# Kernel tuning notes

Hardware: AMD Instinct MI355X
Metric: run time of the kernel (lower is better)

## Reference

```python
import jax, jax.numpy as jnp
import numpy as np

H, C = 4, 32            # heads, per-head out channels -> H*C = 128
NEG = jnp.float32(-1e9) # stand-in for -inf mask (keeps grads finite)
NUM_LOC = 15            # self.num_locations hardcoded to 15


def _tconv(x, src, dst, ea, Wq, bq, Wk, bk, Wv, bv, We, Ws, bs, Wb):
    # PyG TransformerConv(beta=True, concat=True, edge_dim=1)
    N = x.shape[0]
    q = (x @ Wq + bq).reshape(N, H, C)
    k = (x @ Wk + bk).reshape(N, H, C)
    v = (x @ Wv + bv).reshape(N, H, C)
    e = (ea @ We).reshape(-1, H, C)  # edge embedding [E,H,C]
    kj = k[src] + e
    alpha = jnp.einsum('ehc,ehc->eh', q[dst], kj) / jnp.sqrt(jnp.float32(C))
    # scatter-softmax over incoming edges of each dst node
    amax = jax.ops.segment_max(alpha, dst, num_segments=N)
    ex = jnp.exp(alpha - amax[dst])
    den = jax.ops.segment_sum(ex, dst, num_segments=N)
    w = ex / (den[dst] + 1e-16)
    out = jax.ops.segment_sum((v[src] + e) * w[..., None], dst, num_segments=N).reshape(N, H * C)
    xr = x @ Ws + bs  # lin_skip
    beta = jax.nn.sigmoid(jnp.concatenate([out, xr, out - xr], axis=-1) @ Wb)  # [N,1]
    return beta * xr + (1.0 - beta) * out


def _bn(x, g, b):
    # BatchNorm1d in training mode (batch statistics, biased var)
    m = x.mean(0)
    v = ((x - m) ** 2).mean(0)
    return (x - m) * jax.lax.rsqrt(v + 1e-5) * g + b


def _forward_core(fa, edge_index, active_mask):
    (node_type, requests, latency,
     c0_Wq, c0_bq, c0_Wk, c0_bk, c0_Wv, c0_bv, c0_We, c0_Ws, c0_bs, c0_Wb,
     t0_W, t0_b, bn0_g, bn0_b,
     cs_Wq, cs_bq, cs_Wk, cs_bk, cs_Wv, cs_bv, cs_We, cs_Ws, cs_bs, cs_Wb,
     ts_W, ts_b, bns_g, bns_b,
     emb_W1, emb_b1, emb_W2, emb_b2, emb_W3, emb_b3,
     rem_W, rem_b, add_W, add_b) = fa
    src, dst = edge_index[0], edge_index[1]
    ea = latency[:, None]                      # edge_attr [E,1]
    x = jnp.stack([node_type, requests], axis=1)  # [N,2]
    # NetworkGraphEmbeddingConstructor: conv1 + 4 stacked conv/linear/bn blocks
    x = _tconv(x, src, dst, ea, c0_Wq, c0_bq, c0_Wk, c0_bk, c0_Wv, c0_bv, c0_We, c0_Ws, c0_bs, c0_Wb)
    x = _bn(jax.nn.relu(x @ t0_W + t0_b), bn0_g, bn0_b)
    for i in range(4):
        x = _tconv(x, src, dst, ea, cs_Wq[i], cs_bq[i], cs_Wk[i], cs_bk[i], cs_Wv[i], cs_bv[i], cs_We[i], cs_Ws[i], cs_bs[i], cs_Wb[i])
        x = _bn(jax.nn.relu(x @ ts_W[i] + ts_b[i]), bns_g[i], bns_b[i])
    # embedding_transformation MLP
    x = jax.nn.relu(x @ emb_W1 + emb_b1)
    x = jax.nn.relu(x @ emb_W2 + emb_b2)
    x = x @ emb_W3 + emb_b3                    # [N,64]
    # sampling head (batch_index=None branch)
    N = x.shape[0]
    maskf = jnp.where(active_mask == 1, jnp.float32(0.0), NEG)
    loc = jnp.arange(N) < NUM_LOC
    remove_mask = jnp.where(loc, jnp.where(maskf == 0.0, NEG, jnp.float32(0.0)), maskf)
    logits1 = (x @ rem_W + rem_b)[:, 0] + remove_mask
    k1, k2 = jax.random.split(jax.random.key(42))
    a1 = jnp.argmax(logits1 + jax.random.gumbel(k1, (N,), logits1.dtype))  # Categorical sample
    mask2 = maskf.at[a1].set(0.0)
    t = jnp.tanh(x[a1] @ add_W + add_b)        # [64]
    logits2 = x @ t + mask2
    a2 = jnp.argmax(logits2 + jax.random.gumbel(k2, (N,), logits2.dtype))
    log_probs = jnp.stack([jax.nn.log_softmax(logits1)[a1], jax.nn.log_softmax(logits2)[a2]])
    return jnp.stack([logits1, logits2]), jnp.stack([a1, a2]), log_probs


def setup_inputs() -> dict:
    N, E = 50000, 400000
    F, HC, EMB, L = 2, 128, 32, 4
    key = jax.random.key(0)
    kit = iter(jax.random.split(key, 64))
    def w(shape, s=0.1):
        return jax.random.normal(next(kit), shape, jnp.float32) * s
    return {
        'node_type': w((N,), 1.0),
        'requests': jax.random.uniform(next(kit), (N,), jnp.float32),
        'latency': jax.random.uniform(next(kit), (E,), jnp.float32),
        'edge_index': jax.random.randint(next(kit), (2, E), 0, N, jnp.int32),
        'active_mask': jax.random.randint(next(kit), (N,), 0, 2, jnp.int32),
        'c0_Wq': w((F, HC)), 'c0_bq': w((HC,)),
        'c0_Wk': w((F, HC)), 'c0_bk': w((HC,)),
        'c0_Wv': w((F, HC)), 'c0_bv': w((HC,)),
        'c0_We': w((1, HC)),
        'c0_Ws': w((F, HC)), 'c0_bs': w((HC,)),
        'c0_Wb': w((3 * HC, 1)),
        't0_W': w((HC, EMB)), 't0_b': w((EMB,)),
        'bn0_g': jnp.ones((EMB,), jnp.float32), 'bn0_b': jnp.zeros((EMB,), jnp.float32),
        'cs_Wq': w((L, EMB, HC)), 'cs_bq': w((L, HC)),
        'cs_Wk': w((L, EMB, HC)), 'cs_bk': w((L, HC)),
        'cs_Wv': w((L, EMB, HC)), 'cs_bv': w((L, HC)),
        'cs_We': w((L, 1, HC)),
        'cs_Ws': w((L, EMB, HC)), 'cs_bs': w((L, HC)),
        'cs_Wb': w((L, 3 * HC, 1)),
        'ts_W': w((L, HC, EMB)), 'ts_b': w((L, EMB)),
        'bns_g': jnp.ones((L, EMB), jnp.float32), 'bns_b': jnp.zeros((L, EMB), jnp.float32),
        'emb_W1': w((EMB, 128)), 'emb_b1': w((128,)),
        'emb_W2': w((128, 64)), 'emb_b2': w((64,)),
        'emb_W3': w((64, 64)), 'emb_b3': w((64,)),
        'rem_W': w((64, 1)), 'rem_b': w((1,)),
        'add_W': w((64, 64)), 'add_b': w((64,)),
    }


def reference(node_type, requests, latency, edge_index, active_mask,
              c0_Wq, c0_bq, c0_Wk, c0_bk, c0_Wv, c0_bv, c0_We, c0_Ws, c0_bs, c0_Wb,
              t0_W, t0_b, bn0_g, bn0_b,
              cs_Wq, cs_bq, cs_Wk, cs_bk, cs_Wv, cs_bv, cs_We, cs_Ws, cs_bs, cs_Wb,
              ts_W, ts_b, bns_g, bns_b,
              emb_W1, emb_b1, emb_W2, emb_b2, emb_W3, emb_b3,
              rem_W, rem_b, add_W, add_b):
    fa = (node_type, requests, latency,
          c0_Wq, c0_bq, c0_Wk, c0_bk, c0_Wv, c0_bv, c0_We, c0_Ws, c0_bs, c0_Wb,
          t0_W, t0_b, bn0_g, bn0_b,
          cs_Wq, cs_bq, cs_Wk, cs_bk, cs_Wv, cs_bv, cs_We, cs_Ws, cs_bs, cs_Wb,
          ts_W, ts_b, bns_g, bns_b,
          emb_W1, emb_b1, emb_W2, emb_b2, emb_W3, emb_b3,
          rem_W, rem_b, add_W, add_b)
    return _forward_core(fa, edge_index, active_mask)
```

## Files before the change

kernel.cpp:

```cpp
#include <hip/hip_runtime.h>
#include <hip/hip_fp16.h>
#include <cstdint>
#include <math.h>

typedef _Float16 h2 __attribute__((ext_vector_type(2)));

__device__ __forceinline__ h2 f2h2(float a, float b) {
    h2 r; r.x = (_Float16)a; r.y = (_Float16)b; return r;
}
__device__ __forceinline__ float fdot2f(h2 a, h2 b, float c) {
    return __builtin_amdgcn_fdot2(a, b, c, false);
}

union f4h {
    float4 f;
    h2 h[4];
    __half2 u[4];
};

__device__ __forceinline__ uint32_t rotl32(uint32_t x, uint32_t n) {
    return (x << n) | (x >> (32u - n));
}

__device__ __forceinline__ void tf2x32(uint32_t k0, uint32_t k1,
                                       uint32_t x0, uint32_t x1,
                                       uint32_t& o0, uint32_t& o1) {
    uint32_t k2 = k0 ^ k1 ^ 0x1BD11BDAu;
    x0 += k0; x1 += k1;
    x0 += x1; x1 = rotl32(x1, 13); x1 ^= x0;
    x0 += x1; x1 = rotl32(x1, 15); x1 ^= x0;
    x0 += x1; x1 = rotl32(x1, 26); x1 ^= x0;
    x0 += x1; x1 = rotl32(x1, 6);  x1 ^= x0;
    x0 += k1; x1 += k2 + 1u;
    x0 += x1; x1 = rotl32(x1, 17); x1 ^= x0;
    x0 += x1; x1 = rotl32(x1, 29); x1 ^= x0;
    x0 += x1; x1 = rotl32(x1, 16); x1 ^= x0;
    x0 += x1; x1 = rotl32(x1, 24); x1 ^= x0;
    x0 += k2; x1 += k0 + 2u;
    x0 += x1; x1 = rotl32(x1, 13); x1 ^= x0;
    x0 += x1; x1 = rotl32(x1, 15); x1 ^= x0;
    x0 += x1; x1 = rotl32(x1, 26); x1 ^= x0;
    x0 += x1; x1 = rotl32(x1, 6);  x1 ^= x0;
    x0 += k0; x1 += k1 + 3u;
    x0 += x1; x1 = rotl32(x1, 17); x1 ^= x0;
    x0 += x1; x1 = rotl32(x1, 29); x1 ^= x0;
    x0 += x1; x1 = rotl32(x1, 16); x1 ^= x0;
    x0 += x1; x1 = rotl32(x1, 24); x1 ^= x0;
    x0 += k1; x1 += k2 + 4u;
    x0 += x1; x1 = rotl32(x1, 13); x1 ^= x0;
    x0 += x1; x1 = rotl32(x1, 15); x1 ^= x0;
    x0 += x1; x1 = rotl32(x1, 26); x1 ^= x0;
    x0 += x1; x1 = rotl32(x1, 6);  x1 ^= x0;
    x0 += k2; x1 += k0 + 5u;
    o0 = x0; o1 = x1;
}

__device__ float gumbel_at(int n, int which, int N) {
    uint32_t a0, a1, b0, b1;
    tf2x32(0u, 42u, 0u, 2u, a0, a1);
    tf2x32(0u, 42u, 1u, 3u, b0, b1);
    uint32_t gk0 = which ? a1 : a0;
    uint32_t gk1 = which ? b1 : b0;
    int half = N >> 1;
    uint32_t o0, o1, bits;
    if (n < half) { tf2x32(gk0, gk1, (uint32_t)n, (uint32_t)(n + half), o0, o1); bits = o0; }
    else          { tf2x32(gk0, gk1, (uint32_t)(n - half), (uint32_t)n, o0, o1); bits = o1; }
    float f = __uint_as_float((bits >> 9) | 0x3F800000u) - 1.0f;
    float u = fmaxf(1.17549435e-38f, f);
    return -logf(-logf(u));
}

__device__ __forceinline__ uint32_t fmono(float f) {
    uint32_t b = __float_as_uint(f);
    return (b & 0x80000000u) ? ~b : (b | 0x80000000u);
}
__device__ __forceinline__ float funmono(uint32_t u) {
    uint32_t b = (u & 0x80000000u) ? (u & 0x7FFFFFFFu) : ~u;
    return __uint_as_float(b);
}

#define NEGF (-1e9f)
#define ATTNGRID 2048

__global__ void k_hist(const int* __restrict__ dstp, int* __restrict__ deg, int E) {
    int e = blockIdx.x * 256 + threadIdx.x;
    if (e < E) atomicAdd(&deg[dstp[e]], 1);
}

__global__ void k_scan1(const int* __restrict__ deg, int* __restrict__ bsum, int N) {
    __shared__ int s[256];
    int i = blockIdx.x * 256 + threadIdx.x;
    s[threadIdx.x] = (i < N) ? deg[i] : 0;
    __syncthreads();
    for (int st = 128; st > 0; st >>= 1) {
        if (threadIdx.x < st) s[threadIdx.x] += s[threadIdx.x + st];
        __syncthreads();
    }
    if (threadIdx.x == 0) bsum[blockIdx.x] = s[0];
}

__global__ void k_scan2(int* __restrict__ bsum, int nb) {
    __shared__ int s[256];
    int i = threadIdx.x;
    int v = (i < nb) ? bsum[i] : 0;
    s[i] = v;
    __syncthreads();
    for (int st = 1; st < 256; st <<= 1) {
        int t = (i >= st) ? s[i - st] : 0;
        __syncthreads();
        s[i] += t;
        __syncthreads();
    }
    if (i < nb) bsum[i] = s[i] - v;
}

__global__ void k_scan3(const int* __restrict__ deg, const int* __restrict__ bsum,
                        int* __restrict__ rowptr, int* __restrict__ cursor, int N) {
    __shared__ int s[256];
    int i = blockIdx.x * 256 + threadIdx.x;
    int v = (i < N) ? deg[i] : 0;
    s[threadIdx.x] = v;
    __syncthreads();
    for (int st = 1; st < 256; st <<= 1) {
        int t = (threadIdx.x >= st) ? s[threadIdx.x - st] : 0;
        __syncthreads();
        s[threadIdx.x] += t;
        __syncthreads();
    }
    int excl = s[threadIdx.x] - v + bsum[blockIdx.x];
    if (i < N) { rowptr[i] = excl; cursor[i] = excl; }
}

__global__ void k_fill(const int* __restrict__ dstp, const int* __restrict__ srcp,
                       const float* __restrict__ lat, int* __restrict__ cursor,
                       int2* __restrict__ srclat, int E) {
    int e = blockIdx.x * 256 + threadIdx.x;
    if (e < E) {
        int pos = atomicAdd(&cursor[dstp[e]], 1);
        srclat[pos] = make_int2(srcp[e], __float_as_int(lat[e]));
    }
}

__global__ __launch_bounds__(512, 4) void k_qkvr(
        const float* __restrict__ xin, const float* __restrict__ nt,
        const float* __restrict__ rq, int din, int N,
        const float* __restrict__ Wq, const float* __restrict__ bq,
        const float* __restrict__ Wk, const float* __restrict__ bk,
        const float* __restrict__ Wv, const float* __restrict__ bv,
        const float* __restrict__ Ws, const float* __restrict__ bs,
        const double* __restrict__ SUM, const double* __restrict__ SUMSQ,
        const float* __restrict__ bng, const float* __restrict__ bnb,
        int applyBN,
        __half* __restrict__ Q, __half* __restrict__ KV, __half* __restrict__ R) {
    __shared__ h2 w2[4][16 * 128];
    __shared__ float bias[4][128];
    __shared__ h2 xs2[32][17];
    __shared__ float sscale[32], sshift[32];
    int t = threadIdx.x;
    int dpCount = din >> 1;
    for (int i = t; i < dpCount * 128; i += 512) {
        int dp = i >> 7, j = i & 127;
        w2[0][i] = f2h2(Wq[(size_t)(2 * dp) * 128 + j], Wq[(size_t)(2 * dp + 1) * 128 + j]);
        w2[1][i] = f2h2(Wk[(size_t)(2 * dp) * 128 + j], Wk[(size_t)(2 * dp + 1) * 128 + j]);
        w2[2][i] = f2h2(Wv[(size_t)(2 * dp) * 128 + j], Wv[(size_t)(2 * dp + 1) * 128 + j]);
        w2[3][i] = f2h2(Ws[(size_t)(2 * dp) * 128 + j], Ws[(size_t)(2 * dp + 1) * 128 + j]);
    }
    if (t < 128) {
        bias[0][t] = bq[t]; bias[1][t] = bk[t]; bias[2][t] = bv[t]; bias[3][t] = bs[t];
    }
    if (t < 32) {
        if (applyBN) {
            double m = SUM[t] / N;
            double v = SUMSQ[t] / N - m * m;
            float inv = rsqrtf((float)v + 1e-5f);
            float sc = inv * bng[t];
            sscale[t] = sc;
            sshift[t] = bnb[t] - (float)m * sc;
        } else {
            sscale[t] = 1.f; sshift[t] = 0.f;
        }
    }
    int quad = t & 31;
    int sub = t >> 5;
    int dpsh = (din == 32) ? 4 : 0;
    int tiles = (N + 31) >> 5;
    for (int tile = blockIdx.x; tile < tiles; tile += gridDim.x) {
        int base = tile << 5;
        __syncthreads();
        for (int i = t; i < 32 * dpCount; i += 512) {
            int nl = i >> dpsh, dp = i & (dpCount - 1);
            int nn = base + nl;
            float x0 = 0.f, x1 = 0.f;
            if (nn < N) {
                if (din == 2) { x0 = nt[nn]; x1 = rq[nn]; }
                else {
                    x0 = xin[(size_t)nn * din + 2 * dp];
                    x1 = xin[(size_t)nn * din + 2 * dp + 1];
                }
            }
            x0 = x0 * sscale[2 * dp] + sshift[2 * dp];
            x1 = x1 * sscale[2 * dp + 1] + sshift[2 * dp + 1];
            xs2[nl][dp] = f2h2(x0, x1);
        }
        __syncthreads();
        float acc[4][2][4];
#pragma unroll
        for (int m = 0; m < 4; ++m)
#pragma unroll
            for (int k = 0; k < 2; ++k)
#pragma unroll
                for (int c = 0; c < 4; ++c) acc[m][k][c] = bias[m][quad * 4 + c];
        for (int dp = 0; dp < dpCount; ++dp) {
            h2 xv0 = xs2[sub * 2 + 0][dp];
            h2 xv1 = xs2[sub * 2 + 1][dp];
#pragma unroll
            for (int m = 0; m < 4; ++m) {
                const h2* wp = &w2[m][dp * 128 + quad * 4];
                h2 wa = wp[0], wb = wp[1], wc = wp[2], wd = wp[3];
                acc[m][0][0] = fdot2f(xv0, wa, acc[m][0][0]);
                acc[m][0][1] = fdot2f(xv0, wb, acc[m][0][1]);
                acc[m][0][2] = fdot2f(xv0, wc, acc[m][0][2]);
                acc[m][0][3] = fdot2f(xv0, wd, acc[m][0][3]);
                acc[m][1][0] = fdot2f(xv1, wa, acc[m][1][0]);
                acc[m][1][1] = fdot2f(xv1, wb, acc[m][1][1]);
                acc[m][1][2] = fdot2f(xv1, wc, acc[m][1][2]);
                acc[m][1][3] = fdot2f(xv1, wd, acc[m][1][3]);
            }
        }
#pragma unroll
        for (int k = 0; k < 2; ++k) {
            int n = base + sub * 2 + k;
            if (n < N) {
                *(__half2*)&Q[(size_t)n * 128 + quad * 4 + 0] =
                    __floats2half2_rn(acc[0][k][0], acc[0][k][1]);
                *(__half2*)&Q[(size_t)n * 128 + quad * 4 + 2] =
                    __floats2half2_rn(acc[0][k][2], acc[0][k][3]);
                *(__half2*)&KV[(size_t)n * 256 + quad * 4 + 0] =
                    __floats2half2_rn(acc[1][k][0], acc[1][k][1]);
                *(__half2*)&KV[(size_t)n * 256 + quad * 4 + 2] =
                    __floats2half2_rn(acc[1][k][2], acc[1][k][3]);
                *(__half2*)&KV[(size_t)n * 256 + 128 + quad * 4 + 0] =
                    __floats2half2_rn(acc[2][k][0], acc[2][k][1]);
                *(__half2*)&KV[(size_t)n * 256 + 128 + quad * 4 + 2] =
                    __floats2half2_rn(acc[2][k][2], acc[2][k][3]);
                *(__half2*)&R[(size_t)n * 128 + quad * 4 + 0] =
                    __floats2half2_rn(acc[3][k][0], acc[3][k][1]);
                *(__half2*)&R[(size_t)n * 128 + quad * 4 + 2] =
                    __floats2half2_rn(acc[3][k][2], acc[3][k][3]);
            }
        }
    }
}

__global__ __launch_bounds__(256) void k_attn(
        const int2* __restrict__ srclat,
        const __half* __restrict__ Q, const __half* __restrict__ KV,
        const float* __restrict__ We,
        const __half* __restrict__ R, const float* __restrict__ Wb,
        const int* __restrict__ rowptr, const int* __restrict__ deg,
        __half* __restrict__ A, int N) {
    int t = threadIdx.x;
    int wvid = t >> 6;
    int l64 = t & 63;
    int slot = l64 >> 4;
    int lane = l64 & 15;
    const float4 we4a = *(const float4*)&We[lane * 8 + 0];
    const float4 we4b = *(const float4*)&We[lane * 8 + 4];
    h2 weh0 = f2h2(we4a.x, we4a.y), weh1 = f2h2(we4a.z, we4a.w);
    h2 weh2 = f2h2(we4b.x, we4b.y), weh3 = f2h2(we4b.z, we4b.w);
    const float4 wb0a = *(const float4*)&Wb[lane * 8 + 0];
    const float4 wb0b = *(const float4*)&Wb[lane * 8 + 4];
    const float4 wb1a = *(const float4*)&Wb[128 + lane * 8 + 0];
    const float4 wb1b = *(const float4*)&Wb[128 + lane * 8 + 4];
    const float4 wb2a = *(const float4*)&Wb[256 + lane * 8 + 0];
    const float4 wb2b = *(const float4*)&Wb[256 + lane * 8 + 4];
    const float4 f4z = make_float4(0.f, 0.f, 0.f, 0.f);

    int T = gridDim.x * 4;
    int n0 = blockIdx.x * 4 + wvid;

    f4h qh, rh, k0, v0;
    int start = 0, d = 0; float l0 = 0.f;
    f4h pq, pr, pk, pv;
    float pl = 0.f;
    int s1 = 0, d1 = 0;
    int2 psl1 = make_int2(0, 0);
    int s2 = 0, d2 = 0;
    qh.f = f4z; rh.f = f4z; k0.f = f4z; v0.f = f4z;
    pq.f = f4z; pr.f = f4z; pk.f = f4z; pv.f = f4z;

    if (n0 < N) {
        start = rowptr[n0]; d = deg[n0];
        qh.f = *(const float4*)(Q + (size_t)n0 * 128 + lane * 8);
        rh.f = *(const float4*)(R + (size_t)n0 * 128 + lane * 8);
        if (slot < d) {
            int2 sl = srclat[start + slot];
            l0 = __int_as_float(sl.y);
            k0.f = *(const float4*)(KV + (size_t)sl.x * 256 + lane * 8);
            v0.f = *(const float4*)(KV + (size_t)sl.x * 256 + 128 + lane * 8);
        }
        int n1 = n0 + T;
        if (n1 < N) {
            s1 = rowptr[n1]; d1 = deg[n1];
            if (slot < d1) psl1 = srclat[s1 + slot];
        }
        int n2 = n0 + 2 * T;
        if (n2 < N) { s2 = rowptr[n2]; d2 = deg[n2]; }
    }

    for (int n = n0; n < N; n += T) {
        int n1 = n + T, n2 = n + 2 * T, n3 = n + 3 * T;
        int s3 = 0, d3 = 0;
        if (n3 < N) { s3 = rowptr[n3]; d3 = deg[n3]; }
        int2 psl2 = make_int2(0, 0);
        if (n2 < N && slot < d2) psl2 = srclat[s2 + slot];
        pq.f = f4z; pr.f = f4z; pk.f = f4z; pv.f = f4z; pl = 0.f;
        if (n1 < N) {
            pq.f = *(const float4*)(Q + (size_t)n1 * 128 + lane * 8);
            pr.f = *(const float4*)(R + (size_t)n1 * 128 + lane * 8);
            if (slot < d1) {
                pl = __int_as_float(psl1.y);
                pk.f = *(const float4*)(KV + (size_t)psl1.x * 256 + lane * 8);
                pv.f = *(const float4*)(KV + (size_t)psl1.x * 256 + 128 + lane * 8);
            }
        }

        float qwe = fdot2f(qh.h[0], weh0, fdot2f(qh.h[1], weh1,
                    fdot2f(qh.h[2], weh2, fdot2f(qh.h[3], weh3, 0.f))));
        qwe += __shfl_xor(qwe, 1); qwe += __shfl_xor(qwe, 2);

        float m = -INFINITY, den = 0.f, plsum = 0.f;
        float a0 = 0.f, a1 = 0.f, a2 = 0.f, a3 = 0.f;
        float a4 = 0.f, a5 = 0.f, a6 = 0.f, a7 = 0.f;

        int idx = slot;
        bool have = idx < d;
        while (have) {
            int idx2 = idx + 4;
            bool have2 = idx2 < d;
            float l1 = 0.f;
            f4h k1, v1;
            k1.f = f4z; v1.f = f4z;
            if (have2) {
                int2 sl = srclat[start + idx2];
                l1 = __int_as_float(sl.y);
                k1.f = *(const float4*)(KV + (size_t)sl.x * 256 + lane * 8);
                v1.f = *(const float4*)(KV + (size_t)sl.x * 256 + 128 + lane * 8);
            }

            float t0 = fdot2f(qh.h[0], k0.h[0], fdot2f(qh.h[1], k0.h[1],
                       fdot2f(qh.h[2], k0.h[2], fdot2f(qh.h[3], k0.h[3], 0.f))));
            t0 += __shfl_xor(t0, 1); t0 += __shfl_xor(t0, 2);
            float alpha = fmaf(l0, qwe, t0) * 0.17677669529663687f;

            float mn = fmaxf(m, alpha);
            float sc = __expf(m - mn);
            float p = __expf(alpha - mn);
            a0 = a0 * sc + p * (float)v0.h[0].x;
            a1 = a1 * sc + p * (float)v0.h[0].y;
            a2 = a2 * sc + p * (float)v0.h[1].x;
            a3 = a3 * sc + p * (float)v0.h[1].y;
            a4 = a4 * sc + p * (float)v0.h[2].x;
            a5 = a5 * sc + p * (float)v0.h[2].y;
            a6 = a6 * sc + p * (float)v0.h[3].x;
            a7 = a7 * sc + p * (float)v0.h[3].y;
            plsum = plsum * sc + p * l0;
            den = den * sc + p;
            m = mn;

            idx = idx2; l0 = l1;
            k0.f = k1.f; v0.f = v1.f;
            have = have2;
        }

#pragma unroll
        for (int off = 16; off <= 32; off <<= 1) {
            float mo = __shfl_xor(m, off);
            float mn = fmaxf(m, mo);
            float sc = (m == -INFINITY) ? 0.f : __expf(m - mn);
            a0 *= sc; a1 *= sc; a2 *= sc; a3 *= sc;
            a4 *= sc; a5 *= sc; a6 *= sc; a7 *= sc;
            den *= sc; plsum *= sc;
            a0 += __shfl_xor(a0, off); a1 += __shfl_xor(a1, off);
            a2 += __shfl_xor(a2, off); a3 += __shfl_xor(a3, off);
            a4 += __shfl_xor(a4, off); a5 += __shfl_xor(a5, off);
            a6 += __shfl_xor(a6, off); a7 += __shfl_xor(a7, off);
            den += __shfl_xor(den, off); plsum += __shfl_xor(plsum, off);
            m = mn;
        }

        float inv = 1.f / (den + 1e-16f);
        float o0 = fmaf(plsum, we4a.x, a0) * inv;
        float o1 = fmaf(plsum, we4a.y, a1) * inv;
        float o2 = fmaf(plsum, we4a.z, a2) * inv;
        float o3 = fmaf(plsum, we4a.w, a3) * inv;
        float o4 = fmaf(plsum, we4b.x, a4) * inv;
        float o5 = fmaf(plsum, we4b.y, a5) * inv;
        float o6 = fmaf(plsum, we4b.z, a6) * inv;
        float o7 = fmaf(plsum, we4b.w, a7) * inv;

        float2 ra = __half22float2(rh.u[0]);
        float2 rb = __half22float2(rh.u[1]);
        float2 rc = __half22float2(rh.u[2]);
        float2 rd = __half22float2(rh.u[3]);
        float g = o0 * wb0a.x + ra.x * wb1a.x + (o0 - ra.x) * wb2a.x
                + o1 * wb0a.y + ra.y * wb1a.y + (o1 - ra.y) * wb2a.y
                + o2 * wb0a.z + rb.x * wb1a.z + (o2 - rb.x) * wb2a.z
                + o3 * wb0a.w + rb.y * wb1a.w + (o3 - rb.y) * wb2a.w
                + o4 * wb0b.x + rc.x * wb1b.x + (o4 - rc.x) * wb2b.x
                + o5 * wb0b.y + rc.y * wb1b.y + (o5 - rc.y) * wb2b.y
                + o6 * wb0b.z + rd.x * wb1b.z + (o6 - rd.x) * wb2b.z
                + o7 * wb0b.w + rd.y * wb1b.w + (o7 - rd.y) * wb2b.w;
        g += __shfl_xor(g, 1); g += __shfl_xor(g, 2);
        g += __shfl_xor(g, 4); g += __shfl_xor(g, 8);
        float beta = 1.0f / (1.0f + __expf(-g));

        if (slot == 0) {
            float b1 = 1.0f - beta;
            *(__half2*)&A[(size_t)n * 128 + lane * 8 + 0] =
                __floats2half2_rn(beta * ra.x + b1 * o0, beta * ra.y + b1 * o1);
            *(__half2*)&A[(size_t)n * 128 + lane * 8 + 2] =
                __floats2half2_rn(beta * rb.x + b1 * o2, beta * rb.y + b1 * o3);
            *(__half2*)&A[(size_t)n * 128 + lane * 8 + 4] =
                __floats2half2_rn(beta * rc.x + b1 * o4, beta * rc.y + b1 * o5);
            *(__half2*)&A[(size_t)n * 128 + lane * 8 + 6] =
                __floats2half2_rn(beta * rd.x + b1 * o6, beta * rd.y + b1 * o7);
        }

        qh.f = pq.f; rh.f = pr.f; k0.f = pk.f; v0.f = pv.f; l0 = pl;
        start = s1; d = d1;
        s1 = s2; d1 = d2; s2 = s3; d2 = d3;
        psl1 = psl2;
    }
}

__global__ __launch_bounds__(256) void k_linstats(
        const __half* __restrict__ A, const float* __restrict__ tW,
        const float* __restrict__ tb, float* __restrict__ H32,
        double* __restrict__ partials, int N) {
    __shared__ h2 w2l[64 * 32];
    __shared__ float bias[32];
    __shared__ h2 xsT[64][66];
    __shared__ double sp1[4][8][4], sp2[4][8][4];
    int t = threadIdx.x;
    for (int i = t; i < 64 * 32; i += 256) {
        int dp = i >> 5, j = i & 31;
        w2l[i] = f2h2(tW[(size_t)(2 * dp) * 32 + j], tW[(size_t)(2 * dp + 1) * 32 + j]);
    }
    if (t < 32) bias[t] = tb[t];
    int quad = t & 7;
    int sub = t >> 3;
    int base = blockIdx.x << 6;

    __syncthreads();
#pragma unroll
    for (int k = 0; k < 4; ++k) {
        int i = t + 256 * k;
        int nl = i >> 4, g8 = i & 15;
        int n = base + nl;
        h2 hv[4];
        if (n < N) {
            const h2* ap = (const h2*)(A + (size_t)n * 128 + g8 * 8);
            hv[0] = ap[0]; hv[1] = ap[1]; hv[2] = ap[2]; hv[3] = ap[3];
        } else {
            h2 z; z.x = (_Float16)0.f; z.y = (_Float16)0.f;
            hv[0] = z; hv[1] = z; hv[2] = z; hv[3] = z;
        }
        xsT[g8 * 4 + 0][nl] = hv[0];
        xsT[g8 * 4 + 1][nl] = hv[1];
        xsT[g8 * 4 + 2][nl] = hv[2];
        xsT[g8 * 4 + 3][nl] = hv[3];
    }
    __syncthreads();

    float acc[2][4];
#pragma unroll
    for (int k = 0; k < 2; ++k)
#pragma unroll
        for (int c = 0; c < 4; ++c) acc[k][c] = bias[quad * 4 + c];
    for (int dp = 0; dp < 64; ++dp) {
        h2 x0 = xsT[dp][sub * 2 + 0];
        h2 x1 = xsT[dp][sub * 2 + 1];
        const h2* wp = &w2l[dp * 32 + quad * 4];
        h2 wa = wp[0], wb = wp[1], wc = wp[2], wd = wp[3];
        acc[0][0] = fdot2f(x0, wa, acc[0][0]);
        acc[0][1] = fdot2f(x0, wb, acc[0][1]);
        acc[0][2] = fdot2f(x0, wc, acc[0][2]);
        acc[0][3] = fdot2f(x0, wd, acc[0][3]);
        acc[1][0] = fdot2f(x1, wa, acc[1][0]);
        acc[1][1] = fdot2f(x1, wb, acc[1][1]);
        acc[1][2] = fdot2f(x1, wc, acc[1][2]);
        acc[1][3] = fdot2f(x1, wd, acc[1][3]);
    }
    double s1[4] = {0, 0, 0, 0}, s2[4] = {0, 0, 0, 0};
#pragma unroll
    for (int k = 0; k < 2; ++k) {
        int n = base + sub * 2 + k;
        if (n < N) {
            float4 yv;
            yv.x = fmaxf(acc[k][0], 0.f); yv.y = fmaxf(acc[k][1], 0.f);
            yv.z = fmaxf(acc[k][2], 0.f); yv.w = fmaxf(acc[k][3], 0.f);
            *(float4*)&H32[(size_t)n * 32 + quad * 4] = yv;
            s1[0] += yv.x; s1[1] += yv.y; s1[2] += yv.z; s1[3] += yv.w;
            s2[0] += (double)yv.x * yv.x; s2[1] += (double)yv.y * yv.y;
            s2[2] += (double)yv.z * yv.z; s2[3] += (double)yv.w * yv.w;
        }
    }
#pragma unroll
    for (int c = 0; c < 4; ++c) {
        s1[c] += __shfl_xor(s1[c], 8);  s2[c] += __shfl_xor(s2[c], 8);
        s1[c] += __shfl_xor(s1[c], 16); s2[c] += __shfl_xor(s2[c], 16);
        s1[c] += __shfl_xor(s1[c], 32); s2[c] += __shfl_xor(s2[c], 32);
    }
    __syncthreads();
    int wave = t >> 6;
    if ((t & 63) < 8) {
#pragma unroll
        for (int c = 0; c < 4; ++c) { sp1[wave][quad][c] = s1[c]; sp2[wave][quad][c] = s2[c]; }
    }
    __syncthreads();
    if (t < 32) {
        int q = t >> 2, c = t & 3;
        double a1 = 0, a2 = 0;
#pragma unroll
        for (int wv = 0; wv < 4; ++wv) { a1 += sp1[wv][q][c]; a2 += sp2[wv][q][c]; }
        partials[(size_t)blockIdx.x * 64 + t] = a1;
        partials[(size_t)blockIdx.x * 64 + 32 + t] = a2;
    }
}

__global__ void k_statred(const double* __restrict__ partials,
                          double* __restrict__ SUM, double* __restrict__ SUMSQ,
                          int nblocks) {
    __shared__ double s[256];
    int col = blockIdx.x;
    double a = 0;
    for (int b = threadIdx.x; b < nblocks; b += 256)
        a += partials[(size_t)b * 64 + col];
    s[threadIdx.x] = a;
    __syncthreads();
    for (int st = 128; st > 0; st >>= 1) {
        if (threadIdx.x < st) s[threadIdx.x] += s[threadIdx.x + st];
        __syncthreads();
    }
    if (threadIdx.x == 0) {
        if (col < 32) SUM[col] = s[0];
        else SUMSQ[col - 32] = s[0];
    }
}

__global__ __launch_bounds__(256) void k_mlp1(
        const float* __restrict__ H32,
        const double* __restrict__ SUM, const double* __restrict__ SUMSQ,
        const float* __restrict__ bng, const float* __restrict__ bnb,
        const float* __restrict__ W1, const float* __restrict__ b1,
        float* __restrict__ Y1, unsigned int* __restrict__ smallbuf, int N) {
    __shared__ float w1[32 * 128];
    __shared__ float sb1[128];
    __shared__ float sscale[32], sshift[32];
    __shared__ float xs[32][36];
    int t = threadIdx.x;
    if (blockIdx.x == 0 && t < 16) smallbuf[t] = 0u;
    for (int i = t; i < 32 * 128; i += 256) w1[i] = W1[i];
    if (t < 128) sb1[t] = b1[t];
    if (t < 32) {
        double m = SUM[t] / N;
        double v = SUMSQ[t] / N - m * m;
        float inv = rsqrtf((float)v + 1e-5f);
        float sc = inv * bng[t];
        sscale[t] = sc;
        sshift[t] = bnb[t] - (float)m * sc;
    }
    int quad = t & 31, sub = t >> 5;
    int tiles = (N + 31) >> 5;
    for (int tile = blockIdx.x; tile < tiles; tile += gridDim.x) {
        int base = tile << 5;
        __syncthreads();
        {
            int nl = t >> 3, q = t & 7;
            int n = base + nl;
            float4 xv = make_float4(0.f, 0.f, 0.f, 0.f);
            if (n < N) xv = *(const float4*)&H32[(size_t)n * 32 + q * 4];
            xs[nl][q * 4 + 0] = xv.x * sscale[q * 4 + 0] + sshift[q * 4 + 0];
            xs[nl][q * 4 + 1] = xv.y * sscale[q * 4 + 1] + sshift[q * 4 + 1];
            xs[nl][q * 4 + 2] = xv.z * sscale[q * 4 + 2] + sshift[q * 4 + 2];
            xs[nl][q * 4 + 3] = xv.w * sscale[q * 4 + 3] + sshift[q * 4 + 3];
        }
        __syncthreads();
        float a[4][4];
#pragma unroll
        for (int k = 0; k < 4; ++k)
#pragma unroll
            for (int c = 0; c < 4; ++c) a[k][c] = sb1[quad * 4 + c];
        for (int d = 0; d < 32; ++d) {
            float4 w4 = *(const float4*)&w1[d * 128 + quad * 4];
#pragma unroll
            for (int k = 0; k < 4; ++k) {
                float x = xs[sub * 4 + k][d];
                a[k][0] = fmaf(x, w4.x, a[k][0]);
                a[k][1] = fmaf(x, w4.y, a[k][1]);
                a[k][2] = fmaf(x, w4.z, a[k][2]);
                a[k][3] = fmaf(x, w4.w, a[k][3]);
            }
        }
#pragma unroll
        for (int k = 0; k < 4; ++k) {
            int n = base + sub * 4 + k;
            if (n < N) {
                float4 yv;
                yv.x = fmaxf(a[k][0], 0.f); yv.y = fmaxf(a[k][1], 0.f);
                yv.z = fmaxf(a[k][2], 0.f); yv.w = fmaxf(a[k][3], 0.f);
                *(float4*)&Y1[(size_t)n * 128 + quad * 4] = yv;
            }
        }
    }
}

__global__ __launch_bounds__(256) void k_mlp2(
        const float* __restrict__ Y1, const float* __restrict__ W2,
        const float* __restrict__ b2, float* __restrict__ Y2, int N) {
    __shared__ float w2f[128 * 64];
    __shared__ float sb2[64];
    __shared__ float xs[32][132];
    int t = threadIdx.x;
    for (int i = t; i < 128 * 64; i += 256) w2f[i] = W2[i];
    if (t < 64) sb2[t] = b2[t];
    int quad = t & 15, sub = t >> 4;
    int tiles = (N + 31) >> 5;
    for (int tile = blockIdx.x; tile < tiles; tile += gridDim.x) {
        int base = tile << 5;
        __syncthreads();
#pragma unroll
        for (int k = 0; k < 4; ++k) {
            int i = t + 256 * k;
            int nl = i >> 5, q = i & 31;
            int n = base + nl;
            float4 xv = make_float4(0.f, 0.f, 0.f, 0.f);
            if (n < N) xv = *(const float4*)&Y1[(size_t)n * 128 + q * 4];
            *(float4*)&xs[nl][q * 4] = xv;
        }
        __syncthreads();
        float a[2][4];
#pragma unroll
        for (int k = 0; k < 2; ++k)
#pragma unroll
            for (int c = 0; c < 4; ++c) a[k][c] = sb2[quad * 4 + c];
        for (int d = 0; d < 128; ++d) {
            float4 w4 = *(const float4*)&w2f[d * 64 + quad * 4];
#pragma unroll
            for (int k = 0; k < 2; ++k) {
                float x = xs[sub * 2 + k][d];
                a[k][0] = fmaf(x, w4.x, a[k][0]);
                a[k][1] = fmaf(x, w4.y, a[k][1]);
                a[k][2] = fmaf(x, w4.z, a[k][2]);
                a[k][3] = fmaf(x, w4.w, a[k][3]);
            }
        }
#pragma unroll
        for (int k = 0; k < 2; ++k) {
            int n = base + sub * 2 + k;
            if (n < N) {
                float4 yv;
                yv.x = fmaxf(a[k][0], 0.f); yv.y = fmaxf(a[k][1], 0.f);
                yv.z = fmaxf(a[k][2], 0.f); yv.w = fmaxf(a[k][3], 0.f);
                *(float4*)&Y2[(size_t)n * 64 + quad * 4] = yv;
            }
        }
    }
}

__global__ __launch_bounds__(256) void k_mlp3(
        const float* __restrict__ Y2, const float* __restrict__ W3,
        const float* __restrict__ b3, float* __restrict__ X3, int N) {
    __shared__ float w3[64 * 64];
    __shared__ float sb3[64];
    __shared__ float xs[32][68];
    int t = threadIdx.x;
    for (int i = t; i < 64 * 64; i += 256) w3[i] = W3[i];
    if (t < 64) sb3[t] = b3[t];
    int quad = t & 15, sub = t >> 4;
    int tiles = (N + 31) >> 5;
    for (int tile = blockIdx.x; tile < tiles; tile += gridDim.x) {
        int base = tile << 5;
        __syncthreads();
#pragma unroll
        for (int k = 0; k < 2; ++k) {
            int i = t + 256 * k;
            int nl = i >> 4, q = i & 15;
            int n = base + nl;
            float4 xv = make_float4(0.f, 0.f, 0.f, 0.f);
            if (n < N) xv = *(const float4*)&Y2[(size_t)n * 64 + q * 4];
            *(float4*)&xs[nl][q * 4] = xv;
        }
        __syncthreads();
        float a[2][4];
#pragma unroll
        for (int k = 0; k < 2; ++k)
#pragma unroll
            for (int c = 0; c < 4; ++c) a[k][c] = sb3[quad * 4 + c];
        for (int d = 0; d < 64; ++d) {
            float4 w4 = *(const float4*)&w3[d * 64 + quad * 4];
#pragma unroll
            for (int k = 0; k < 2; ++k) {
                float x = xs[sub * 2 + k][d];
                a[k][0] = fmaf(x, w4.x, a[k][0]);
                a[k][1] = fmaf(x, w4.y, a[k][1]);
                a[k][2] = fmaf(x, w4.z, a[k][2]);
                a[k][3] = fmaf(x, w4.w, a[k][3]);
            }
        }
#pragma unroll
        for (int k = 0; k < 2; ++k) {
            int n = base + sub * 2 + k;
            if (n < N)
                *(float4*)&X3[(size_t)n * 64 + quad * 4] = *(float4*)a[k];
        }
    }
}

__global__ void k_head1(const float* __restrict__ X3, const float* __restrict__ remW,
                        const float* __restrict__ remB, const int* __restrict__ active,
                        float* __restrict__ l1out, unsigned long long* __restrict__ slot1,
                        unsigned int* __restrict__ m1, int N) {
    int n = blockIdx.x * 256 + threadIdx.x;
    if (n >= N) return;
    const float* xr = X3 + (size_t)n * 64;
    float acc = remB[0];
    for (int d = 0; d < 64; d++) acc = fmaf(xr[d], remW[d], acc);
    float maskf = (active[n] == 1) ? 0.f : NEGF;
    float rm = (n < 15) ? ((maskf == 0.f) ? NEGF : 0.f) : maskf;
    float l1 = acc + rm;
    l1out[n] = l1;
    atomicMax(m1, fmono(l1));
    float z = l1 + gumbel_at(n, 0, N);
    unsigned long long p = ((unsigned long long)fmono(z) << 32) |
                           (unsigned long long)(0xFFFFFFFFu - (unsigned)n);
    atomicMax(slot1, p);
}

__global__ void k_head2(const float* __restrict__ X3, const float* __restrict__ addW,
                        const float* __restrict__ addB,
                        const unsigned long long* __restrict__ slot1,
                        float* __restrict__ tvec, int* __restrict__ a1buf) {
    int j = threadIdx.x;
    unsigned long long p = *slot1;
    int a1 = (int)(0xFFFFFFFFu - (unsigned)(p & 0xFFFFFFFFull));
    const float* xr = X3 + (size_t)a1 * 64;
    float acc = addB[j];
    for (int d = 0; d < 64; d++) acc = fmaf(xr[d], addW[d * 64 + j], acc);
    tvec[j] = tanhf(acc);
    if (j == 0) *a1buf = a1;
}

__global__ void k_head3(const float* __restrict__ X3, const float* __restrict__ tvec,
                        const int* __restrict__ active, const int* __restrict__ a1buf,
                        float* __restrict__ l2out, unsigned long long* __restrict__ slot2,
                        unsigned int* __restrict__ m2, int N) {
    int n = blockIdx.x * 256 + threadIdx.x;
    if (n >= N) return;
    const float* xr = X3 + (size_t)n * 64;
    float acc = 0.f;
    for (int d = 0; d < 64; d++) acc = fmaf(xr[d], tvec[d], acc);
    float maskf = (active[n] == 1) ? 0.f : NEGF;
    if (n == *a1buf) maskf = 0.f;
    float l2 = acc + maskf;
    l2out[n] = l2;
    atomicMax(m2, fmono(l2));
    float z = l2 + gumbel_at(n, 1, N);
    unsigned long long p = ((unsigned long long)fmono(z) << 32) |
                           (unsigned long long)(0xFFFFFFFFu - (unsigned)n);
    atomicMax(slot2, p);
}

__global__ void k_sumexp(const float* __restrict__ l1, const float* __restrict__ l2,
                         const unsigned int* __restrict__ m1, const unsigned int* __restrict__ m2,
                         float* __restrict__ se, int N) {
    int t = blockIdx.x * 256 + threadIdx.x;
    float M1 = funmono(*m1), M2 = funmono(*m2);
    float e1 = 0.f, e2 = 0.f;
    if (t < N) { e1 = expf(l1[t] - M1); e2 = expf(l2[t] - M2); }
    __shared__ float r1[256], r2[256];
    r1[threadIdx.x] = e1; r2[threadIdx.x] = e2;
    __syncthreads();
    for (int s = 128; s > 0; s >>= 1) {
        if (threadIdx.x < s) { r1[threadIdx.x] += r1[threadIdx.x + s]; r2[threadIdx.x] += r2[threadIdx.x + s]; }
        __syncthreads();
    }
    if (threadIdx.x == 0) { atomicAdd(&se[0], r1[0]); atomicAdd(&se[1], r2[0]); }
}

__global__ void k_final(const float* __restrict__ l1, const float* __restrict__ l2,
                        const unsigned long long* __restrict__ slot2,
                        const int* __restrict__ a1buf,
                        const unsigned int* __restrict__ m1, const unsigned int* __restrict__ m2,
                        const float* __restrict__ se, float* __restrict__ outTail, int N) {
    int a1 = *a1buf;
    int a2 = (int)(0xFFFFFFFFu - (unsigned)((*slot2) & 0xFFFFFFFFull));
    outTail[0] = (float)a1;
    outTail[1] = (float)a2;
    outTail[2] = l1[a1] - (funmono(*m1) + logf(se[0]));
    outTail[3] = l2[a2] - (funmono(*m2) + logf(se[1]));
}

extern "C" void kernel_launch(void* const* d_in, const int* in_sizes, int n_in,
                              void* d_out, int out_size, void* d_ws, size_t ws_size,
                              hipStream_t stream) {
    const float* node_type = (const float*)d_in[0];
    const float* requests  = (const float*)d_in[1];
    const float* latency   = (const float*)d_in[2];
    const int* edge_index  = (const int*)d_in[3];
    const int* active      = (const int*)d_in[4];
    int N = in_sizes[0];
    int E = in_sizes[2];
    const int* src = edge_index;
    const int* dst = edge_index + E;
    float* out = (float*)d_out;

    char* base = (char*)d_ws;
    size_t off = 0;
    auto alloc = [&](size_t bytes) -> char* {
        char* p = base + off;
        off += (bytes + 255) & ~(size_t)255;
        return p;
    };
    char* Abuf   = alloc((size_t)N * 128 * 4);
    char* Qbuf   = alloc((size_t)N * 128 * 4);
    __half* KV   = (__half*)alloc((size_t)N * 256 * 2);
    char* Rbuf   = alloc((size_t)N * 128 * 4);
    float* H32   = (float*)alloc((size_t)N * 32 * 4);
    int* deg     = (int*)alloc((size_t)N * 4);
    int* rowptr  = (int*)alloc((size_t)N * 4);
    int* cursor  = (int*)alloc((size_t)N * 4);
    int2* srclat = (int2*)alloc((size_t)E * 8);
    int* bsum    = (int*)alloc(1024 * 4);
    int lsTiles = (N + 63) / 64;
    double* partials = (double*)alloc((size_t)lsTiles * 64 * 8);
    double* SUM  = (double*)alloc(512);
    double* SUMSQ = SUM + 32;
    char* small  = alloc(1024);
    unsigned long long* slot1 = (unsigned long long*)small;
    unsigned long long* slot2 = slot1 + 1;
    unsigned int* m1 = (unsigned int*)(small + 16);
    unsigned int* m2 = m1 + 1;
    float* se = (float*)(small + 24);
    int* a1buf = (int*)(small + 32);
    float* tvec = (float*)(small + 64);

    __half* Ah = (__half*)Abuf;   float* Y2f = (float*)Abuf;
    __half* Qh = (__half*)Qbuf;   float* Y1f = (float*)Qbuf;
    __half* Rh = (__half*)Rbuf;   float* X3f = (float*)Rbuf;

    int ng = (N + 255) / 256;
    int egE = (E + 255) / 256;
    int nb = ng;

    (void)hipMemsetAsync(deg, 0, (size_t)N * 4, stream);
    k_hist<<<egE, 256, 0, stream>>>(dst, deg, E);
    k_scan1<<<nb, 256, 0, stream>>>(deg, bsum, N);
    k_scan2<<<1, 256, 0, stream>>>(bsum, nb);
    k_scan3<<<nb, 256, 0, stream>>>(deg, bsum, rowptr, cursor, N);
    k_fill<<<egE, 256, 0, stream>>>(dst, src, latency, cursor, srclat, E);

    for (int L = 0; L < 5; ++L) {
        int din = L ? 32 : 2;
        const float* xin = L ? H32 : nullptr;
        const float* Wq = L ? (const float*)d_in[19] + (size_t)(L - 1) * 4096 : (const float*)d_in[5];
        const float* bq = L ? (const float*)d_in[20] + (size_t)(L - 1) * 128  : (const float*)d_in[6];
        const float* Wk = L ? (const float*)d_in[21] + (size_t)(L - 1) * 4096 : (const float*)d_in[7];
        const float* bk = L ? (const float*)d_in[22] + (size_t)(L - 1) * 128  : (const float*)d_in[8];
        const float* Wv = L ? (const float*)d_in[23] + (size_t)(L - 1) * 4096 : (const float*)d_in[9];
        const float* bv = L ? (const float*)d_in[24] + (size_t)(L - 1) * 128  : (const float*)d_in[10];
        const float* We = L ? (const float*)d_in[25] + (size_t)(L - 1) * 128  : (const float*)d_in[11];
        const float* Ws = L ? (const float*)d_in[26] + (size_t)(L - 1) * 4096 : (const float*)d_in[12];
        const float* bs = L ? (const float*)d_in[27] + (size_t)(L - 1) * 128  : (const float*)d_in[13];
        const float* Wb = L ? (const float*)d_in[28] + (size_t)(L - 1) * 384  : (const float*)d_in[14];
        const float* tW = L ? (const float*)d_in[29] + (size_t)(L - 1) * 4096 : (const float*)d_in[15];
        const float* tb = L ? (const float*)d_in[30] + (size_t)(L - 1) * 32   : (const float*)d_in[16];
        const float* bngP = (L == 1) ? (const float*)d_in[17]
                          : (L >= 2) ? (const float*)d_in[31] + (size_t)(L - 2) * 32 : nullptr;
        const float* bnbP = (L == 1) ? (const float*)d_in[18]
                          : (L >= 2) ? (const float*)d_in[32] + (size_t)(L - 2) * 32 : nullptr;

        k_qkvr<<<1024, 512, 0, stream>>>(xin, node_type, requests, din, N,
                                         Wq, bq, Wk, bk, Wv, bv, Ws, bs,
                                         SUM, SUMSQ, bngP, bnbP, (L > 0) ? 1 : 0,
                                         Qh, KV, Rh);
        k_attn<<<ATTNGRID, 256, 0, stream>>>(srclat, Qh, KV, We, Rh, Wb,
                                             rowptr, deg, Ah, N);
        k_linstats<<<lsTiles, 256, 0, stream>>>(Ah, tW, tb, H32, partials, N);
        k_statred<<<64, 256, 0, stream>>>(partials, SUM, SUMSQ, lsTiles);
    }

    k_mlp1<<<512, 256, 0, stream>>>(H32, SUM, SUMSQ,
                                    (const float*)d_in[31] + 3 * 32,
                                    (const float*)d_in[32] + 3 * 32,
                                    (const float*)d_in[33], (const float*)d_in[34],
                                    Y1f, (unsigned int*)small, N);
    k_mlp2<<<512, 256, 0, stream>>>(Y1f, (const float*)d_in[35], (const float*)d_in[36],
                                    Y2f, N);
    k_mlp3<<<512, 256, 0, stream>>>(Y2f, (const float*)d_in[37], (const float*)d_in[38],
                                    X3f, N);
    k_head1<<<ng, 256, 0, stream>>>(X3f, (const float*)d_in[39], (const float*)d_in[40],
                                    active, out, slot1, m1, N);
    k_head2<<<1, 64, 0, stream>>>(X3f, (const float*)d_in[41], (const float*)d_in[42],
                                  slot1, tvec, a1buf);
    k_head3<<<ng, 256, 0, stream>>>(X3f, tvec, active, a1buf, out + N, slot2, m2, N);
    k_sumexp<<<ng, 256, 0, stream>>>(out, out + N, m1, m2, se, N);
    k_final<<<1, 1, 0, stream>>>(out, out + N, slot2, a1buf, m1, m2, se, out + 2 * N, N);
}
```

Measured before the change: 732.2 us.

## Replace batchnorm stat reduction kernel with atomics and pack attention math into float2

The separate k_statred kernel and its partials buffer are removed. k_linstats now atomically adds per-block double sums straight into SUM/SUMSQ, and k_attn zeroes those accumulators at start. Five launches are saved, at the cost of contended double atomics and an order-dependent sum. In the attention kernel, the beta gate weights are pre-folded in shared memory (Wb0+Wb2, Wb1-Wb2), the accumulators use float2 vectors that may map to packed FP32 instructions, and redundant zero-initialisations are dropped.

```diff
diff --git a/kernel.cpp b/kernel.cpp
--- a/kernel.cpp
+++ b/kernel.cpp
@@ -4,6 +4,7 @@
 #include <math.h>
 
 typedef _Float16 h2 __attribute__((ext_vector_type(2)));
+typedef float f32x2 __attribute__((ext_vector_type(2)));
 
 __device__ __forceinline__ h2 f2h2(float a, float b) {
     h2 r; r.x = (_Float16)a; r.y = (_Float16)b; return r;
@@ -11,6 +12,11 @@
 __device__ __forceinline__ float fdot2f(h2 a, h2 b, float c) {
     return __builtin_amdgcn_fdot2(a, b, c, false);
 }
+__device__ __forceinline__ f32x2 bc2(float x) { f32x2 r; r.x = x; r.y = x; return r; }
+__device__ __forceinline__ f32x2 cvt2(h2 v) {
+    f32x2 r; r.x = (float)v.x; r.y = (float)v.y; return r;
+}
+__device__ __forceinline__ f32x2 mk2(float a, float b) { f32x2 r; r.x = a; r.y = b; return r; }
 
 union f4h {
     float4 f;
@@ -258,22 +264,31 @@
         const float* __restrict__ We,
         const __half* __restrict__ R, const float* __restrict__ Wb,
         const int* __restrict__ rowptr, const int* __restrict__ deg,
-        __half* __restrict__ A, int N) {
+        __half* __restrict__ A, double* __restrict__ statz, int N) {
+    __shared__ float weL[128], wboL[128], wbrL[128];
     int t = threadIdx.x;
+    if (blockIdx.x == 0 && t < 64) statz[t] = 0.0;
+    if (t < 128) {
+        float w0 = Wb[t], w1 = Wb[128 + t], w2v = Wb[256 + t];
+        weL[t] = We[t];
+        wboL[t] = w0 + w2v;
+        wbrL[t] = w1 - w2v;
+    }
+    __syncthreads();
+
     int wvid = t >> 6;
     int l64 = t & 63;
     int slot = l64 >> 4;
     int lane = l64 & 15;
-    const float4 we4a = *(const float4*)&We[lane * 8 + 0];
-    const float4 we4b = *(const float4*)&We[lane * 8 + 4];
-    h2 weh0 = f2h2(we4a.x, we4a.y), weh1 = f2h2(we4a.z, we4a.w);
-    h2 weh2 = f2h2(we4b.x, we4b.y), weh3 = f2h2(we4b.z, we4b.w);
-    const float4 wb0a = *(const float4*)&Wb[lane * 8 + 0];
-    const float4 wb0b = *(const float4*)&Wb[lane * 8 + 4];
-    const float4 wb1a = *(const float4*)&Wb[128 + lane * 8 + 0];
-    const float4 wb1b = *(const float4*)&Wb[128 + lane * 8 + 4];
-    const float4 wb2a = *(const float4*)&Wb[256 + lane * 8 + 0];
-    const float4 wb2b = *(const float4*)&Wb[256 + lane * 8 + 4];
+    const f32x2* wep = (const f32x2*)&weL[lane * 8];
+    const f32x2* bop = (const f32x2*)&wboL[lane * 8];
+    const f32x2* brp = (const f32x2*)&wbrL[lane * 8];
+    h2 weh0, weh1, weh2, weh3;
+    {
+        f32x2 wa = wep[0], wb = wep[1], wc = wep[2], wd = wep[3];
+        weh0 = f2h2(wa.x, wa.y); weh1 = f2h2(wb.x, wb.y);
+        weh2 = f2h2(wc.x, wc.y); weh3 = f2h2(wd.x, wd.y);
+    }
     const float4 f4z = make_float4(0.f, 0.f, 0.f, 0.f);
 
     int T = gridDim.x * 4;
@@ -314,7 +329,6 @@
         if (n3 < N) { s3 = rowptr[n3]; d3 = deg[n3]; }
         int2 psl2 = make_int2(0, 0);
         if (n2 < N && slot < d2) psl2 = srclat[s2 + slot];
-        pq.f = f4z; pr.f = f4z; pk.f = f4z; pv.f = f4z; pl = 0.f;
         if (n1 < N) {
             pq.f = *(const float4*)(Q + (size_t)n1 * 128 + lane * 8);
             pr.f = *(const float4*)(R + (size_t)n1 * 128 + lane * 8);
@@ -330,8 +344,7 @@
         qwe += __shfl_xor(qwe, 1); qwe += __shfl_xor(qwe, 2);
 
         float m = -INFINITY, den = 0.f, plsum = 0.f;
-        float a0 = 0.f, a1 = 0.f, a2 = 0.f, a3 = 0.f;
-        float a4 = 0.f, a5 = 0.f, a6 = 0.f, a7 = 0.f;
+        f32x2 A0 = bc2(0.f), A1 = bc2(0.f), A2 = bc2(0.f), A3 = bc2(0.f);
 
         int idx = slot;
         bool have = idx < d;
@@ -340,7 +353,6 @@
             bool have2 = idx2 < d;
             float l1 = 0.f;
             f4h k1, v1;
-            k1.f = f4z; v1.f = f4z;
             if (have2) {
                 int2 sl = srclat[start + idx2];
                 l1 = __int_as_float(sl.y);
@@ -356,16 +368,13 @@
             float mn = fmaxf(m, alpha);
             float sc = __expf(m - mn);
             float p = __expf(alpha - mn);
-            a0 = a0 * sc + p * (float)v0.h[0].x;
-            a1 = a1 * sc + p * (float)v0.h[0].y;
-            a2 = a2 * sc + p * (float)v0.h[1].x;
-            a3 = a3 * sc + p * (float)v0.h[1].y;
-            a4 = a4 * sc + p * (float)v0.h[2].x;
-            a5 = a5 * sc + p * (float)v0.h[2].y;
-            a6 = a6 * sc + p * (float)v0.h[3].x;
-            a7 = a7 * sc + p * (float)v0.h[3].y;
+            f32x2 sc2 = bc2(sc), p2 = bc2(p);
+            A0 = A0 * sc2 + p2 * cvt2(v0.h[0]);
+            A1 = A1 * sc2 + p2 * cvt2(v0.h[1]);
+            A2 = A2 * sc2 + p2 * cvt2(v0.h[2]);
+            A3 = A3 * sc2 + p2 * cvt2(v0.h[3]);
             plsum = plsum * sc + p * l0;
-            den = den * sc + p;
+            den = fmaf(den, sc, p);
             m = mn;
 
             idx = idx2; l0 = l1;
@@ -378,53 +387,46 @@
             float mo = __shfl_xor(m, off);
             float mn = fmaxf(m, mo);
             float sc = (m == -INFINITY) ? 0.f : __expf(m - mn);
-            a0 *= sc; a1 *= sc; a2 *= sc; a3 *= sc;
-            a4 *= sc; a5 *= sc; a6 *= sc; a7 *= sc;
+            f32x2 sc2 = bc2(sc);
+            A0 *= sc2; A1 *= sc2; A2 *= sc2; A3 *= sc2;
             den *= sc; plsum *= sc;
-            a0 += __shfl_xor(a0, off); a1 += __shfl_xor(a1, off);
-            a2 += __shfl_xor(a2, off); a3 += __shfl_xor(a3, off);
-            a4 += __shfl_xor(a4, off); a5 += __shfl_xor(a5, off);
-            a6 += __shfl_xor(a6, off); a7 += __shfl_xor(a7, off);
+            A0 += mk2(__shfl_xor(A0.x, off), __shfl_xor(A0.y, off));
+            A1 += mk2(__shfl_xor(A1.x, off), __shfl_xor(A1.y, off));
+            A2 += mk2(__shfl_xor(A2.x, off), __shfl_xor(A2.y, off));
+            A3 += mk2(__shfl_xor(A3.x, off), __shfl_xor(A3.y, off));
             den += __shfl_xor(den, off); plsum += __shfl_xor(plsum, off);
             m = mn;
         }
 
         float inv = 1.f / (den + 1e-16f);
-        float o0 = fmaf(plsum, we4a.x, a0) * inv;
-        float o1 = fmaf(plsum, we4a.y, a1) * inv;
-        float o2 = fmaf(plsum, we4a.z, a2) * inv;
-        float o3 = fmaf(plsum, we4a.w, a3) * inv;
-        float o4 = fmaf(plsum, we4b.x, a4) * inv;
-        float o5 = fmaf(plsum, we4b.y, a5) * inv;
-        float o6 = fmaf(plsum, we4b.z, a6) * inv;
-        float o7 = fmaf(plsum, we4b.w, a7) * inv;
-
-        float2 ra = __half22float2(rh.u[0]);
-        float2 rb = __half22float2(rh.u[1]);
-        float2 rc = __half22float2(rh.u[2]);
-        float2 rd = __half22float2(rh.u[3]);
-        float g = o0 * wb0a.x + ra.x * wb1a.x + (o0 - ra.x) * wb2a.x
-                + o1 * wb0a.y + ra.y * wb1a.y + (o1 - ra.y) * wb2a.y
-                + o2 * wb0a.z + rb.x * wb1a.z + (o2 - rb.x) * wb2a.z
-                + o3 * wb0a.w + rb.y * wb1a.w + (o3 - rb.y) * wb2a.w
-                + o4 * wb0b.x + rc.x * wb1b.x + (o4 - rc.x) * wb2b.x
-                + o5 * wb0b.y + rc.y * wb1b.y + (o5 - rc.y) * wb2b.y
-                + o6 * wb0b.z + rd.x * wb1b.z + (o6 - rd.x) * wb2b.z
-                + o7 * wb0b.w + rd.y * wb1b.w + (o7 - rd.y) * wb2b.w;
+        f32x2 inv2 = bc2(inv), pls2 = bc2(plsum);
+        f32x2 O0 = (A0 + pls2 * wep[0]) * inv2;
+        f32x2 O1 = (A1 + pls2 * wep[1]) * inv2;
+        f32x2 O2 = (A2 + pls2 * wep[2]) * inv2;
+        f32x2 O3 = (A3 + pls2 * wep[3]) * inv2;
+
+        f32x2 R0 = cvt2(rh.h[0]), R1 = cvt2(rh.h[1]);
+        f32x2 R2 = cvt2(rh.h[2]), R3 = cvt2(rh.h[3]);
+        f32x2 G = O0 * bop[0];
+        G += R0 * brp[0];
+        G += O1 * bop[1]; G += R1 * brp[1];
+        G += O2 * bop[2]; G += R2 * brp[2];
+        G += O3 * bop[3]; G += R3 * brp[3];
+        float g = G.x + G.y;
         g += __shfl_xor(g, 1); g += __shfl_xor(g, 2);
         g += __shfl_xor(g, 4); g += __shfl_xor(g, 8);
         float beta = 1.0f / (1.0f + __expf(-g));
 
         if (slot == 0) {
-            float b1 = 1.0f - beta;
-            *(__half2*)&A[(size_t)n * 128 + lane * 8 + 0] =
-                __floats2half2_rn(beta * ra.x + b1 * o0, beta * ra.y + b1 * o1);
-            *(__half2*)&A[(size_t)n * 128 + lane * 8 + 2] =
-                __floats2half2_rn(beta * rb.x + b1 * o2, beta * rb.y + b1 * o3);
-            *(__half2*)&A[(size_t)n * 128 + lane * 8 + 4] =
-                __floats2half2_rn(beta * rc.x + b1 * o4, beta * rc.y + b1 * o5);
-            *(__half2*)&A[(size_t)n * 128 + lane * 8 + 6] =
-                __floats2half2_rn(beta * rd.x + b1 * o6, beta * rd.y + b1 * o7);
+            f32x2 bb = bc2(beta), ib = bc2(1.0f - beta);
+            f32x2 W0 = bb * R0 + ib * O0;
+            f32x2 W1 = bb * R1 + ib * O1;
+            f32x2 W2 = bb * R2 + ib * O2;
+            f32x2 W3 = bb * R3 + ib * O3;
+            *(__half2*)&A[(size_t)n * 128 + lane * 8 + 0] = __floats2half2_rn(W0.x, W0.y);
+            *(__half2*)&A[(size_t)n * 128 + lane * 8 + 2] = __floats2half2_rn(W1.x, W1.y);
+            *(__half2*)&A[(size_t)n * 128 + lane * 8 + 4] = __floats2half2_rn(W2.x, W2.y);
+            *(__half2*)&A[(size_t)n * 128 + lane * 8 + 6] = __floats2half2_rn(W3.x, W3.y);
         }
 
         qh.f = pq.f; rh.f = pr.f; k0.f = pk.f; v0.f = pv.f; l0 = pl;
@@ -437,7 +439,7 @@
 __global__ __launch_bounds__(256) void k_linstats(
         const __half* __restrict__ A, const float* __restrict__ tW,
         const float* __restrict__ tb, float* __restrict__ H32,
-        double* __restrict__ partials, int N) {
+        double* __restrict__ statbuf, int N) {
     __shared__ h2 w2l[64 * 32];
     __shared__ float bias[32];
     __shared__ h2 xsT[64][66];
@@ -524,28 +526,8 @@
         double a1 = 0, a2 = 0;
 #pragma unroll
         for (int wv = 0; wv < 4; ++wv) { a1 += sp1[wv][q][c]; a2 += sp2[wv][q][c]; }
-        partials[(size_t)blockIdx.x * 64 + t] = a1;
-        partials[(size_t)blockIdx.x * 64 + 32 + t] = a2;
-    }
-}
-
-__global__ void k_statred(const double* __restrict__ partials,
-                          double* __restrict__ SUM, double* __restrict__ SUMSQ,
-                          int nblocks) {
-    __shared__ double s[256];
-    int col = blockIdx.x;
-    double a = 0;
-    for (int b = threadIdx.x; b < nblocks; b += 256)
-        a += partials[(size_t)b * 64 + col];
-    s[threadIdx.x] = a;
-    __syncthreads();
-    for (int st = 128; st > 0; st >>= 1) {
-        if (threadIdx.x < st) s[threadIdx.x] += s[threadIdx.x + st];
-        __syncthreads();
-    }
-    if (threadIdx.x == 0) {
-        if (col < 32) SUM[col] = s[0];
-        else SUMSQ[col - 32] = s[0];
+        unsafeAtomicAdd(&statbuf[t], a1);
+        unsafeAtomicAdd(&statbuf[32 + t], a2);
     }
 }
 
@@ -833,8 +815,6 @@
     int* cursor  = (int*)alloc((size_t)N * 4);
     int2* srclat = (int2*)alloc((size_t)E * 8);
     int* bsum    = (int*)alloc(1024 * 4);
-    int lsTiles = (N + 63) / 64;
-    double* partials = (double*)alloc((size_t)lsTiles * 64 * 8);
     double* SUM  = (double*)alloc(512);
     double* SUMSQ = SUM + 32;
     char* small  = alloc(1024);
@@ -853,6 +833,7 @@
     int ng = (N + 255) / 256;
     int egE = (E + 255) / 256;
     int nb = ng;
+    int lsTiles = (N + 63) / 64;
 
     (void)hipMemsetAsync(deg, 0, (size_t)N * 4, stream);
     k_hist<<<egE, 256, 0, stream>>>(dst, deg, E);
@@ -886,9 +867,8 @@
                                          SUM, SUMSQ, bngP, bnbP, (L > 0) ? 1 : 0,
                                          Qh, KV, Rh);
         k_attn<<<ATTNGRID, 256, 0, stream>>>(srclat, Qh, KV, We, Rh, Wb,
-                                             rowptr, deg, Ah, N);
-        k_linstats<<<lsTiles, 256, 0, stream>>>(Ah, tW, tb, H32, partials, N);
-        k_statred<<<64, 256, 0, stream>>>(partials, SUM, SUMSQ, lsTiles);
+                                             rowptr, deg, Ah, SUM, N);
+        k_linstats<<<lsTiles, 256, 0, stream>>>(Ah, tW, tb, H32, SUM, N);
     }
 
     k_mlp1<<<512, 256, 0, stream>>>(H32, SUM, SUMSQ,
```

New measurement: 765.0 us. 4.5% more time.
